# Kernel tuning notes

Hardware: AMD Instinct MI355X
Metric: run time of the kernel (lower is better)

The kernel has to match this reference:

```python
import jax, jax.numpy as jnp
import numpy as np

DIM = 128
H = 8
NEG_SLOPE = 0.2
SCALE = 12.0
N_ITEMS = 81920
E_INT = 163840
N_T = 4096
NUM_NODE = 40000


def _normalize(x, eps=1e-12):
    n = jnp.linalg.norm(x, axis=-1, keepdims=True)
    return x / jnp.maximum(n, eps)


def _gat(feat, src, dst, fc_w, attn_l, attn_r, bias):
    # GATConv with residual (Identity, since in_feats == out_feats) and bias.
    N = feat.shape[0]
    fs = (feat @ fc_w.T).reshape(N, H, DIM)                # [N,H,D]
    el = jnp.einsum('nhd,hd->nh', fs, attn_l)              # [N,H]
    er = jnp.einsum('nhd,hd->nh', fs, attn_r)              # [N,H]
    e = el[src] + er[dst]                                  # u_add_v -> [E,H]
    e = jnp.where(e >= 0, e, NEG_SLOPE * e)                # leaky_relu
    # edge_softmax grouped by destination node
    emax = jax.ops.segment_max(e, dst, num_segments=N)
    ex = jnp.exp(e - emax[dst])
    denom = jax.ops.segment_sum(ex, dst, num_segments=N)
    a = ex / denom[dst]                                    # [E,H]
    # u_mul_e + sum aggregation
    m = fs[src] * a[:, :, None]                            # [E,H,D]
    rst = jax.ops.segment_sum(m, dst, num_segments=N)      # [N,H,D]
    rst = rst + feat[:, None, :] + bias.reshape(1, H, DIM)
    return rst


def setup_inputs() -> dict:
    key = jax.random.key(0)
    ks = jax.random.split(key, 20)
    stdv = 1.0 / np.sqrt(DIM)

    def unif(k, shape):
        return jax.random.uniform(k, shape, jnp.float32, -stdv, stdv)

    return {
        'iid': jax.random.randint(ks[0], (N_ITEMS,), 0, NUM_NODE),
        'tid': jax.random.randint(ks[1], (N_T,), 0, 10),
        'pid': jax.random.randint(ks[2], (N_ITEMS,), 0, 200),
        'src_i': jax.random.randint(ks[3], (E_INT,), 0, N_ITEMS),
        'dst_i': jax.random.randint(ks[4], (E_INT,), 0, N_ITEMS),
        'agg_src': jnp.arange(N_ITEMS),
        'agg_dst': jnp.sort(jax.random.randint(ks[5], (N_ITEMS,), 0, N_T)),
        'last_nodes': jax.random.randint(ks[6], (N_T,), 0, N_ITEMS),
        'emb': unif(ks[7], (NUM_NODE, DIM)),
        'pos_emb': unif(ks[8], (200, DIM)),
        'target_emb': unif(ks[9], (10, DIM)),
        'gat1_fc': unif(ks[10], (H * DIM, DIM)),
        'gat1_al': unif(ks[11], (H, DIM)),
        'gat1_ar': unif(ks[12], (H, DIM)),
        'gat1_b': jnp.zeros((H * DIM,), jnp.float32),
        'gat2_fc': unif(ks[13], (H * DIM, DIM)),
        'gat2_al': unif(ks[14], (H, DIM)),
        'gat2_ar': unif(ks[15], (H, DIM)),
        'gat2_b': jnp.zeros((H * DIM,), jnp.float32),
        'q_w': unif(ks[16], (DIM, 2 * DIM)),
        'fc_sr_w': unif(ks[17], (DIM, 2 * DIM)),
    }


def reference(iid, tid, pid, src_i, dst_i, agg_src, agg_dst, last_nodes,
              emb, pos_emb, target_emb,
              gat1_fc, gat1_al, gat1_ar, gat1_b,
              gat2_fc, gat2_al, gat2_ar, gat2_b,
              q_w, fc_sr_w):
    h_v = _normalize(emb[iid])                              # [N_items, D]
    h_p = pos_emb[pid]                                      # [E_agg, D]
    h_t = target_emb[tid]                                   # [N_T, D]

    # gat1 on interacts; gat2 on reversed interacts; max over heads each
    h1 = _gat(h_v, src_i, dst_i, gat1_fc, gat1_al, gat1_ar, gat1_b).max(axis=1)
    h2 = _gat(h_v, dst_i, src_i, gat2_fc, gat2_al, gat2_ar, gat2_b).max(axis=1)
    h = _normalize(h1 + h2)                                 # [N_items, D]

    # PosAggregator over 'agg' edges (item -> target)
    ft = h[agg_src]                                         # [E_agg, D]
    e = jnp.tanh(jnp.concatenate([ft, h_p], axis=-1) @ q_w.T)
    w = jnp.sum(e * h_t[agg_dst], axis=-1, keepdims=True)   # udf_agg weight
    sr_g = jax.ops.segment_sum(ft * w, agg_dst, num_segments=h_t.shape[0])
    sr_l = h[last_nodes]                                    # last-item features

    sr = jnp.concatenate([sr_g, sr_l], axis=-1) @ fc_sr_w.T
    scores = SCALE * (_normalize(sr) @ _normalize(emb).T)   # [N_T, num_node]
    return scores
```

## Files before the change

kernel.cpp:

```cpp
#include <hip/hip_runtime.h>
#include <stdint.h>

#define DD 128
#define HN 8
#define NITEMS 81920
#define EINT 163840
#define NT 4096
#define NV 40000
#define NVPAD 40064
#define EAGG 81920
#define NEG_SLOPE 0.2f
#define SCALE 12.0f

typedef unsigned short u16;
typedef __attribute__((ext_vector_type(8))) short bf16x8;
typedef __attribute__((ext_vector_type(4))) float f32x4;
typedef __attribute__((ext_vector_type(4))) unsigned short u16x4;

__device__ __forceinline__ float bf2f(unsigned short u){ return __uint_as_float(((unsigned)u)<<16); }
__device__ __forceinline__ unsigned short f2bf(float f){
  unsigned u = __float_as_uint(f);
  u += 0x7fffu + ((u>>16)&1u);
  return (unsigned short)(u>>16);
}

__global__ __launch_bounds__(256) void k_cast3(const float* __restrict__ fc1, const float* __restrict__ fc2,
    const float* __restrict__ qw, const float* __restrict__ fcsr,
    u16* __restrict__ w1, u16* __restrict__ w2, u16* __restrict__ qb, float* __restrict__ fT){
  int i = blockIdx.x*256 + threadIdx.x;
  if (i < 131072) w1[i] = f2bf(fc1[i]);
  else if (i < 262144) w2[i-131072] = f2bf(fc2[i-131072]);
  else if (i < 294912) qb[i-262144] = f2bf(qw[i-262144]);
  else if (i < 327680){
    int j = i - 294912;
    int k = j >> 7, col = j & 127;
    fT[j] = fcsr[(size_t)col*256 + k];
  }
}

__global__ __launch_bounds__(128) void k_prep_u(const float* __restrict__ fc1, const float* __restrict__ al1,
    const float* __restrict__ ar1, const float* __restrict__ fc2, const float* __restrict__ al2,
    const float* __restrict__ ar2, u16* __restrict__ U){
  int r = blockIdx.x, k = threadIdx.x;
  if (r >= 32){ U[(size_t)r*DD + k] = 0; return; }
  int g = r>>3, h = r&7;
  const float* fc = (g>=2)? fc2 : fc1;
  const float* av = (g==0)? al1 : (g==1)? ar1 : (g==2)? al2 : ar2;
  float s = 0.f;
  for (int d=0; d<DD; ++d) s += fc[(size_t)(h*DD+d)*DD + k] * av[h*DD+d];
  U[(size_t)r*DD + k] = f2bf(s);
}

__global__ __launch_bounds__(256) void k_norm(const float* __restrict__ emb, const int* __restrict__ iid,
    u16* __restrict__ nemb, u16* __restrict__ hvb, int* __restrict__ cnt){
  int gi = blockIdx.x*256 + threadIdx.x;
  if (gi < 2*NITEMS) cnt[gi] = 0;
  int w = gi >> 6;
  int lane = gi & 63;
  u16* dst; const float* src;
  if (w < NVPAD){
    dst = nemb + (size_t)w*DD;
    if (w >= NV){ dst[lane*2]=0; dst[lane*2+1]=0; return; }
    src = emb + (size_t)w*DD;
  } else {
    int n = w - NVPAD;
    dst = hvb + (size_t)n*DD;
    src = emb + (size_t)iid[n]*DD;
  }
  float2 v = *(const float2*)(src + lane*2);
  float ss = v.x*v.x + v.y*v.y;
  #pragma unroll
  for (int m=1;m<64;m<<=1) ss += __shfl_xor(ss, m);
  float inv = 1.f / fmaxf(sqrtf(ss), 1e-12f);
  dst[lane*2]   = f2bf(v.x*inv);
  dst[lane*2+1] = f2bf(v.y*inv);
}

template<int OUT_BF16>
__global__ __launch_bounds__(256) void gemm_nt(const u16* __restrict__ A, const u16* __restrict__ B,
                                               void* __restrict__ C, int M, int N, int K,
                                               float alpha, int ldc, int nvalid){
  __shared__ u16 As[128*32];
  __shared__ u16 Bs[128*32];
  int m0 = blockIdx.x*128, n0 = blockIdx.y*128;
  int t = threadIdx.x, lane = t&63, wid = t>>6;
  int wm = wid>>1, wn = wid&1;
  f32x4 zero = {0.f,0.f,0.f,0.f};
  f32x4 acc[4][4];
  #pragma unroll
  for (int i=0;i<4;i++)
    #pragma unroll
    for (int j=0;j<4;j++) acc[i][j] = zero;
  int lr = lane & 15, lk = (lane>>4)*8;
  for (int k0=0; k0<K; k0+=32){
    #pragma unroll
    for (int cc=0; cc<2; ++cc){
      int c = t + cc*256;
      int row = c>>2, col = (c&3)*8;
      *(bf16x8*)(void*)&As[c*8] = *(const bf16x8*)(const void*)&A[(size_t)(m0+row)*K + k0 + col];
      *(bf16x8*)(void*)&Bs[c*8] = *(const bf16x8*)(const void*)&B[(size_t)(n0+row)*K + k0 + col];
    }
    __syncthreads();
    bf16x8 af[4], bfr[4];
    #pragma unroll
    for (int m=0;m<4;m++) af[m]  = *(const bf16x8*)(const void*)&As[(wm*64+m*16+lr)*32 + lk];
    #pragma unroll
    for (int n=0;n<4;n++) bfr[n] = *(const bf16x8*)(const void*)&Bs[(wn*64+n*16+lr)*32 + lk];
    #pragma unroll
    for (int m=0;m<4;m++)
      #pragma unroll
      for (int n=0;n<4;n++)
        acc[m][n] = __builtin_amdgcn_mfma_f32_16x16x32_bf16(af[m], bfr[n], acc[m][n], 0,0,0);
    __syncthreads();
  }
  #pragma unroll
  for (int m=0;m<4;m++)
    #pragma unroll
    for (int n=0;n<4;n++)
      #pragma unroll
      for (int r=0;r<4;r++){
        int row = m0 + wm*64 + m*16 + (lane>>4)*4 + r;
        int col = n0 + wn*64 + n*16 + (lane&15);
        if (col < nvalid){
          float v = acc[m][n][r]*alpha;
          if (OUT_BF16) ((u16*)C)[(size_t)row*ldc + col] = f2bf(v);
          else          ((float*)C)[(size_t)row*ldc + col] = v;
        }
      }
}

__global__ __launch_bounds__(256) void k_deg2(const int* __restrict__ di, const int* __restrict__ si,
                                              int* __restrict__ cnt){
  int i = blockIdx.x*256+threadIdx.x;
  if (i<EINT){ atomicAdd(&cnt[di[i]],1); atomicAdd(&cnt[NITEMS+si[i]],1); }
}

__global__ __launch_bounds__(256) void k_scan_a(int* cnt, int* off, int* bsum, int n){
  __shared__ int buf[256];
  int b = blockIdx.x, t = threadIdx.x, i = b*256+t;
  int v = (i<n)? cnt[i] : 0;
  buf[t] = v; __syncthreads();
  #pragma unroll
  for (int ofs=1; ofs<256; ofs<<=1){
    int x = (t>=ofs)? buf[t-ofs] : 0;
    __syncthreads();
    buf[t] += x;
    __syncthreads();
  }
  if (i<n){ off[i] = buf[t]-v; cnt[i] = 0; }
  if (t==255) bsum[b] = buf[255];
}

__global__ __launch_bounds__(1024) void k_scan_b(int* bsum, int* off, int nb, int n){
  __shared__ int buf[1024];
  int t = threadIdx.x;
  int v = (t<nb)? bsum[t] : 0;
  buf[t]=v; __syncthreads();
  #pragma unroll
  for (int ofs=1; ofs<1024; ofs<<=1){
    int x=(t>=ofs)?buf[t-ofs]:0; __syncthreads(); buf[t]+=x; __syncthreads();
  }
  if (t<nb) bsum[t] = buf[t]-v;
  if (t==1023) off[n] = buf[1023];
}

__global__ __launch_bounds__(256) void k_scan_c(int* __restrict__ off, const int* __restrict__ bsum, int n){
  int i = blockIdx.x*256+threadIdx.x;
  if (i<n) off[i] += bsum[blockIdx.x];
}

__global__ __launch_bounds__(256) void k_scatter2(const int* __restrict__ di, const int* __restrict__ si,
    const int* __restrict__ off, int* __restrict__ cnt, int* __restrict__ sid){
  int i = blockIdx.x*256+threadIdx.x;
  if (i<EINT){
    int a = di[i];         sid[off[a]+atomicAdd(&cnt[a],1)] = si[i];
    int b = NITEMS+si[i];  sid[off[b]+atomicAdd(&cnt[b],1)] = di[i];
  }
}

__global__ __launch_bounds__(256) void k_aw(const int* __restrict__ off, const int* __restrict__ sid,
    const float* __restrict__ ecat, u16* __restrict__ aw){
  int u = blockIdx.x*256 + threadIdx.x;
  if (u >= 2*NITEMS) return;
  int g = (u >= NITEMS) ? 1 : 0;
  int w = u - g*NITEMS;
  int cl = g*16, cr = g*16 + 8;
  float ern[8];
  #pragma unroll
  for (int h=0;h<8;h++) ern[h] = ecat[(size_t)w*32 + cr + h];
  int lo = off[u], hi = off[u+1];
  float den[8];
  #pragma unroll
  for (int h=0;h<8;h++) den[h] = 0.f;
  for (int i=lo;i<hi;++i){
    const float* e = ecat + (size_t)sid[i]*32 + cl;
    #pragma unroll
    for (int h=0;h<8;h++){
      float lv = e[h] + ern[h];
      lv = (lv>=0.f)? lv : NEG_SLOPE*lv;
      den[h] += expf(lv);
    }
  }
  float inv[8];
  #pragma unroll
  for (int h=0;h<8;h++) inv[h] = (den[h]>0.f)? 1.f/den[h] : 0.f;
  for (int i=lo;i<hi;++i){
    const float* e = ecat + (size_t)sid[i]*32 + cl;
    bf16x8 o;
    #pragma unroll
    for (int h=0;h<8;h++){
      float lv = e[h] + ern[h];
      lv = (lv>=0.f)? lv : NEG_SLOPE*lv;
      o[h] = (short)f2bf(expf(lv)*inv[h]);
    }
    *(bf16x8*)(void*)&aw[(size_t)i*8] = o;
  }
}

__global__ __launch_bounds__(512) void k_gatfuse(const int* __restrict__ off, const int* __restrict__ sid,
    const u16* __restrict__ aw, const u16* __restrict__ hvb,
    const u16* __restrict__ wfc1, const u16* __restrict__ wfc2,
    const float* __restrict__ b1, const float* __restrict__ b2,
    u16* __restrict__ hb){
  __shared__ __align__(16) char smem[64*DD*4];
  u16* aggS = (u16*)smem;
  float* F = (float*)smem;
  int n0 = blockIdx.x*64;
  int t = threadIdx.x, lane = t&63, wid = t>>6;
  int lr = lane&15, lq = lane>>4;
  int nd = t>>3, dch = t&7;
  float rm[2][4][4];
  #pragma unroll
  for (int g=0;g<2;g++)
    #pragma unroll
    for (int m=0;m<4;m++)
      #pragma unroll
      for (int r=0;r<4;r++) rm[g][m][r] = -1e30f;

  #pragma unroll
  for (int g=0; g<2; ++g){
    const u16* wfc = g ? wfc2 : wfc1;
    const float* bias = g ? b2 : b1;
    int u = g*NITEMS + n0 + nd;
    int lo = off[u], hi = off[u+1];
    #pragma unroll
    for (int hp=0; hp<4; ++hp){
      float a0[16], a1[16];
      #pragma unroll
      for (int j=0;j<16;j++){ a0[j]=0.f; a1[j]=0.f; }
      for (int i=lo; i<hi; ++i){
        int s = sid[i];
        bf16x8 v0 = *(const bf16x8*)(const void*)&hvb[(size_t)s*DD + dch*16];
        bf16x8 v1 = *(const bf16x8*)(const void*)&hvb[(size_t)s*DD + dch*16 + 8];
        unsigned wp = *(const unsigned*)(const void*)&aw[(size_t)i*8 + 2*hp];
        float w0 = bf2f((u16)(wp & 0xffffu)), w1 = bf2f((u16)(wp >> 16));
        #pragma unroll
        for (int j=0;j<8;j++){
          float f0 = bf2f((u16)v0[j]);
          float f1 = bf2f((u16)v1[j]);
          a0[j] += w0*f0; a0[8+j] += w0*f1;
          a1[j] += w1*f0; a1[8+j] += w1*f1;
        }
      }
      #pragma unroll
      for (int sub=0; sub<2; ++sub){
        int h = 2*hp + sub;
        const float* ap = sub ? a1 : a0;
        __syncthreads();
        {
          bf16x8 o0, o1;
          #pragma unroll
          for (int j=0;j<8;j++){ o0[j] = (short)f2bf(ap[j]); o1[j] = (short)f2bf(ap[8+j]); }
          *(bf16x8*)(void*)&aggS[nd*DD + (((dch*2)   ^ (nd&7))*8)] = o0;
          *(bf16x8*)(void*)&aggS[nd*DD + (((dch*2+1) ^ (nd&7))*8)] = o1;
        }
        __syncthreads();
        f32x4 acc[4];
        #pragma unroll
        for (int m=0;m<4;m++){ f32x4 z={0.f,0.f,0.f,0.f}; acc[m]=z; }
        #pragma unroll
        for (int ks=0; ks<4; ++ks){
          bf16x8 bfr = *(const bf16x8*)(const void*)&wfc[(size_t)(h*DD + wid*16 + lr)*DD + ks*32 + lq*8];
          #pragma unroll
          for (int m=0;m<4;m++){
            int row = m*16 + lr;
            bf16x8 af = *(const bf16x8*)(const void*)&aggS[row*DD + ((((ks*4+lq) ^ (row&7)))*8)];
            acc[m] = __builtin_amdgcn_mfma_f32_16x16x32_bf16(af, bfr, acc[m], 0,0,0);
          }
        }
        float bn = bias[h*DD + wid*16 + lr];
        #pragma unroll
        for (int m=0;m<4;m++)
          #pragma unroll
          for (int r=0;r<4;r++)
            rm[g][m][r] = fmaxf(rm[g][m][r], acc[m][r] + bn);
      }
    }
  }
  __syncthreads();
  #pragma unroll
  for (int m=0;m<4;m++)
    #pragma unroll
    for (int r=0;r<4;r++){
      int row = m*16 + lq*4 + r;
      int col = wid*16 + lr;
      float hvv = bf2f(hvb[(size_t)(n0+row)*DD + col]);
      F[row*DD + col] = rm[0][m][r] + rm[1][m][r] + 2.f*hvv;
    }
  __syncthreads();
  {
    int r8 = t>>3, q = t&7;
    float ss = 0.f;
    #pragma unroll
    for (int j=0;j<16;j+=4){
      float4 v4 = *(const float4*)&F[r8*DD + q*16 + j];
      ss += v4.x*v4.x + v4.y*v4.y + v4.z*v4.z + v4.w*v4.w;
    }
    ss += __shfl_xor(ss,1); ss += __shfl_xor(ss,2); ss += __shfl_xor(ss,4);
    float inv = 1.f/fmaxf(sqrtf(ss),1e-12f);
    #pragma unroll
    for (int j=0;j<16;j+=4){
      float4 v4 = *(const float4*)&F[r8*DD + q*16 + j];
      u16x4 o = {f2bf(v4.x*inv), f2bf(v4.y*inv), f2bf(v4.z*inv), f2bf(v4.w*inv)};
      *(u16x4*)(void*)&hb[(size_t)(n0+r8)*DD + q*16 + j] = o;
    }
  }
}

__global__ __launch_bounds__(256) void k_epw(const int* __restrict__ asrc, const int* __restrict__ pid,
    const int* __restrict__ adst, const int* __restrict__ tid_, const u16* __restrict__ hb,
    const float* __restrict__ pemb, const u16* __restrict__ qwb, const float* __restrict__ temb,
    float* __restrict__ wv){
  __shared__ u16 As[128*32];
  __shared__ u16 Bs[128*32];
  __shared__ float tembS[10*DD];
  __shared__ float wsum[128];
  __shared__ int rowtt[128];
  int m0 = blockIdx.x*128;
  int t = threadIdx.x, lane = t&63, wid = t>>6;
  int wm = wid>>1, wn = wid&1, lr = lane&15, lq = lane>>4;
  for (int i=t; i<10*DD; i+=256) tembS[i] = temb[i];
  if (t < 128){ rowtt[t] = tid_[adst[m0+t]]; wsum[t] = 0.f; }
  f32x4 zero = {0.f,0.f,0.f,0.f};
  f32x4 acc[4][4];
  #pragma unroll
  for (int i=0;i<4;i++)
    #pragma unroll
    for (int j=0;j<4;j++) acc[i][j] = zero;
  for (int k0=0; k0<256; k0+=32){
    #pragma unroll
    for (int cc=0; cc<2; ++cc){
      int c = t + cc*256;
      int row = c>>2;
      int kk = k0 + (c&3)*8;
      bf16x8 av;
      if (k0 < 128){
        av = *(const bf16x8*)(const void*)&hb[(size_t)asrc[m0+row]*DD + kk];
      } else {
        const float* p = pemb + (size_t)pid[m0+row]*DD + (kk-128);
        float4 p0 = *(const float4*)p;
        float4 p1 = *(const float4*)(p+4);
        av[0]=(short)f2bf(p0.x); av[1]=(short)f2bf(p0.y); av[2]=(short)f2bf(p0.z); av[3]=(short)f2bf(p0.w);
        av[4]=(short)f2bf(p1.x); av[5]=(short)f2bf(p1.y); av[6]=(short)f2bf(p1.z); av[7]=(short)f2bf(p1.w);
      }
      *(bf16x8*)(void*)&As[c*8] = av;
      *(bf16x8*)(void*)&Bs[c*8] = *(const bf16x8*)(const void*)&qwb[(size_t)row*256 + kk];
    }
    __syncthreads();
    bf16x8 af[4], bfr[4];
    #pragma unroll
    for (int m=0;m<4;m++) af[m]  = *(const bf16x8*)(const void*)&As[(wm*64+m*16+lr)*32 + lq*8];
    #pragma unroll
    for (int n=0;n<4;n++) bfr[n] = *(const bf16x8*)(const void*)&Bs[(wn*64+n*16+lr)*32 + lq*8];
    #pragma unroll
    for (int m=0;m<4;m++)
      #pragma unroll
      for (int n=0;n<4;n++)
        acc[m][n] = __builtin_amdgcn_mfma_f32_16x16x32_bf16(af[m], bfr[n], acc[m][n], 0,0,0);
    __syncthreads();
  }
  #pragma unroll
  for (int m=0;m<4;m++)
    #pragma unroll
    for (int r=0;r<4;r++){
      int lrow = wm*64 + m*16 + lq*4 + r;
      int tt = rowtt[lrow];
      float p = 0.f;
      #pragma unroll
      for (int n=0;n<4;n++){
        int col = wn*64 + n*16 + lr;
        p += tanhf(acc[m][n][r]) * tembS[tt*DD + col];
      }
      #pragma unroll
      for (int msk=1; msk<16; msk<<=1) p += __shfl_xor(p, msk);
      if (lr==0) atomicAdd(&wsum[lrow], p);
    }
  __syncthreads();
  if (t < 128) wv[m0+t] = wsum[t];
}

__device__ __forceinline__ int lbound(const int* a, int n, int key){
  int lo=0, hi=n;
  while (lo<hi){ int mid=(lo+hi)>>1; if (a[mid]<key) lo=mid+1; else hi=mid; }
  return lo;
}

__global__ __launch_bounds__(256) void k_sr(const u16* __restrict__ hb, const float* __restrict__ w,
    const int* __restrict__ asrc, const int* __restrict__ adst, const int* __restrict__ lastn,
    const float* __restrict__ fcsrT, u16* __restrict__ nsr){
  __shared__ float cat[256];
  __shared__ float red[128];
  __shared__ int lohi[2];
  int t = blockIdx.x, tid = threadIdx.x;
  if (tid == 0){ lohi[0] = lbound(adst, EAGG, t); lohi[1] = lbound(adst, EAGG, t+1); }
  __syncthreads();
  int lo = lohi[0], hi = lohi[1];
  if (tid < DD){
    float a = 0.f;
    for (int i=lo;i<hi;++i) a += bf2f(hb[(size_t)asrc[i]*DD + tid]) * w[i];
    cat[tid] = a;
  } else {
    int d = tid - DD;
    cat[DD + d] = bf2f(hb[(size_t)lastn[t]*DD + d]);
  }
  __syncthreads();
  float s = 0.f;
  if (tid < DD){
    #pragma unroll 8
    for (int k=0;k<256;++k) s += cat[k]*fcsrT[(size_t)k*DD + tid];
    red[tid] = s*s;
  }
  __syncthreads();
  for (int st=64; st>0; st>>=1){
    if (tid < st) red[tid] += red[tid+st];
    __syncthreads();
  }
  if (tid < DD){
    float inv = 1.f/fmaxf(sqrtf(red[0]),1e-12f);
    nsr[(size_t)t*DD + tid] = f2bf(s*inv);
  }
}

__global__ __launch_bounds__(256) void gemm_sc(const u16* __restrict__ A, const u16* __restrict__ B,
                                               float* __restrict__ C){
  __shared__ __align__(16) char smem[16384];
  u16* As = (u16*)smem;
  u16* Bs = As + 4096;
  float* tr = (float*)smem;
  int flat = blockIdx.y*gridDim.x + blockIdx.x;
  int nf = (flat&7)*1252 + (flat>>3);
  int m0 = (nf & 31)*128;
  int n0 = (nf >> 5)*128;
  int t = threadIdx.x, lane = t&63, wid = t>>6;
  int wm = wid>>1, wn = wid&1, lr = lane&15, lq = lane>>4;
  f32x4 zero = {0.f,0.f,0.f,0.f};
  f32x4 acc[4][4];
  #pragma unroll
  for (int i=0;i<4;i++)
    #pragma unroll
    for (int j=0;j<4;j++) acc[i][j] = zero;
  for (int k0=0; k0<DD; k0+=32){
    #pragma unroll
    for (int cc=0; cc<2; ++cc){
      int c = t + cc*256;
      int row = c>>2, col = (c&3)*8;
      *(bf16x8*)(void*)&As[c*8] = *(const bf16x8*)(const void*)&A[(size_t)(m0+row)*DD + k0 + col];
      *(bf16x8*)(void*)&Bs[c*8] = *(const bf16x8*)(const void*)&B[(size_t)(n0+row)*DD + k0 + col];
    }
    __syncthreads();
    bf16x8 af[4], bfr[4];
    #pragma unroll
    for (int m=0;m<4;m++) af[m]  = *(const bf16x8*)(const void*)&As[(wm*64+m*16+lr)*32 + lq*8];
    #pragma unroll
    for (int n=0;n<4;n++) bfr[n] = *(const bf16x8*)(const void*)&Bs[(wn*64+n*16+lr)*32 + lq*8];
    #pragma unroll
    for (int m=0;m<4;m++)
      #pragma unroll
      for (int n=0;n<4;n++)
        acc[m][n] = __builtin_amdgcn_mfma_f32_16x16x32_bf16(af[m], bfr[n], acc[m][n], 0,0,0);
    __syncthreads();
  }
  #pragma unroll
  for (int m=0;m<4;m++){
    #pragma unroll
    for (int n=0;n<4;n++)
      #pragma unroll
      for (int r=0;r<4;r++)
        tr[wid*1024 + (lq*4+r)*64 + n*16 + lr] = acc[m][n][r]*SCALE;
    __syncthreads();
    int row16 = lane>>2, ch = (lane&3)*16;
    int grow = m0 + wm*64 + m*16 + row16;
    int gcol = n0 + wn*64 + ch;
    if (gcol < NV){
      const float* s = &tr[wid*1024 + row16*64 + ch];
      float* d = &C[(size_t)grow*NV + gcol];
      *(float4*)(d)    = *(const float4*)(s);
      *(float4*)(d+4)  = *(const float4*)(s+4);
      *(float4*)(d+8)  = *(const float4*)(s+8);
      *(float4*)(d+12) = *(const float4*)(s+12);
    }
    __syncthreads();
  }
}

extern "C" void kernel_launch(void* const* d_in, const int* in_sizes, int n_in,
                              void* d_out, int out_size, void* d_ws, size_t ws_size,
                              hipStream_t stream){
  (void)in_sizes; (void)n_in; (void)out_size; (void)ws_size;
  const int*   iid   = (const int*)d_in[0];
  const int*   tid_  = (const int*)d_in[1];
  const int*   pid   = (const int*)d_in[2];
  const int*   src_i = (const int*)d_in[3];
  const int*   dst_i = (const int*)d_in[4];
  const int*   asrc  = (const int*)d_in[5];
  const int*   adst  = (const int*)d_in[6];
  const int*   lastn = (const int*)d_in[7];
  const float* emb   = (const float*)d_in[8];
  const float* pemb  = (const float*)d_in[9];
  const float* temb  = (const float*)d_in[10];
  const float* fc1   = (const float*)d_in[11];
  const float* al1   = (const float*)d_in[12];
  const float* ar1   = (const float*)d_in[13];
  const float* b1    = (const float*)d_in[14];
  const float* fc2   = (const float*)d_in[15];
  const float* al2   = (const float*)d_in[16];
  const float* ar2   = (const float*)d_in[17];
  const float* b2    = (const float*)d_in[18];
  const float* qw    = (const float*)d_in[19];
  const float* fcsr  = (const float*)d_in[20];

  char* ws = (char*)d_ws;
  size_t o = 0;
  auto alc = [&](size_t b)->char*{ char* r = ws + o; o += (b + 511) & ~(size_t)511; return r; };
  u16*   hvb  = (u16*)  alc((size_t)NITEMS*DD*2);
  u16*   hb   = (u16*)  alc((size_t)NITEMS*DD*2);
  float* ecat = (float*)alc((size_t)NITEMS*32*4);
  int*   off  = (int*)  alc((size_t)(2*NITEMS+1)*4);
  int*   cnt  = (int*)  alc((size_t)(2*NITEMS)*4);
  int*   bsum = (int*)  alc((size_t)1024*4);
  int*   sid  = (int*)  alc((size_t)(2*EINT)*4);
  u16*   aw   = (u16*)  alc((size_t)(2*EINT)*8*2);
  u16*   wfc1 = (u16*)  alc((size_t)1024*DD*2);
  u16*   wfc2 = (u16*)  alc((size_t)1024*DD*2);
  u16*   qwb  = (u16*)  alc((size_t)DD*256*2);
  float* fT   = (float*)alc((size_t)256*DD*4);
  u16*   Umat = (u16*)  alc((size_t)128*DD*2);
  float* wv   = (float*)alc((size_t)EAGG*4);
  u16*   nsr  = (u16*)  alc((size_t)NT*DD*2);
  u16*   nemb = (u16*)  alc((size_t)NVPAD*DD*2);

  const int N2 = 2*NITEMS;
  const int NB2 = N2/256;

  k_norm<<<(NVPAD+NITEMS)/4, 256, 0, stream>>>(emb, iid, nemb, hvb, cnt);
  k_prep_u<<<128, 128, 0, stream>>>(fc1, al1, ar1, fc2, al2, ar2, Umat);
  k_cast3<<<1280, 256, 0, stream>>>(fc1, fc2, qw, fcsr, wfc1, wfc2, qwb, fT);
  gemm_nt<0><<<dim3(NITEMS/128, 1), 256, 0, stream>>>(hvb, Umat, ecat, NITEMS, 128, DD, 1.f, 32, 32);

  k_deg2<<<(EINT+255)/256, 256, 0, stream>>>(dst_i, src_i, cnt);
  k_scan_a<<<NB2, 256, 0, stream>>>(cnt, off, bsum, N2);
  k_scan_b<<<1, 1024, 0, stream>>>(bsum, off, NB2, N2);
  k_scan_c<<<NB2, 256, 0, stream>>>(off, bsum, N2);
  k_scatter2<<<(EINT+255)/256, 256, 0, stream>>>(dst_i, src_i, off, cnt, sid);

  k_aw<<<N2/256, 256, 0, stream>>>(off, sid, ecat, aw);

  k_gatfuse<<<NITEMS/64, 512, 0, stream>>>(off, sid, aw, hvb, wfc1, wfc2, b1, b2, hb);

  k_epw<<<EAGG/128, 256, 0, stream>>>(asrc, pid, adst, tid_, hb, pemb, qwb, temb, wv);
  k_sr<<<NT, 256, 0, stream>>>(hb, wv, asrc, adst, lastn, fT, nsr);

  gemm_sc<<<dim3(32, NVPAD/128), 256, 0, stream>>>(nsr, nemb, (float*)d_out);
}
```

Before: 674.3 us.

## Gather all heads in one edge pass and halve node tile in fused GAT kernel

The fused GAT kernel now walks each node's edge list once per graph, accumulating all 8 heads together, instead of re-walking it once per head pair (four passes). Per-head aggregates are staged into a padded shared buffer for all heads at once, so the per-head sync pairs disappear. The block tile drops from 64 to 32 nodes with 16 threads per node, doubling the grid. The cost is a larger per-thread accumulator (64 floats), more shared memory and more reloads of weight fragments across blocks.

```diff
diff --git a/kernel.cpp b/kernel.cpp
--- a/kernel.cpp
+++ b/kernel.cpp
@@ -222,108 +222,107 @@
     const u16* __restrict__ wfc1, const u16* __restrict__ wfc2,
     const float* __restrict__ b1, const float* __restrict__ b2,
     u16* __restrict__ hb){
-  __shared__ __align__(16) char smem[64*DD*4];
-  u16* aggS = (u16*)smem;
-  float* F = (float*)smem;
-  int n0 = blockIdx.x*64;
+  __shared__ __align__(16) u16 S[8*32*136];
+  float* F = (float*)S;
+  const int TS = 32*136;
+  int n0 = blockIdx.x*32;
   int t = threadIdx.x, lane = t&63, wid = t>>6;
   int lr = lane&15, lq = lane>>4;
-  int nd = t>>3, dch = t&7;
-  float rm[2][4][4];
+  int nd = t>>4, dch = t&15;
+  int elo[2], ehi[2];
+  #pragma unroll
+  for (int g=0; g<2; ++g){
+    int u = g*NITEMS + n0 + nd;
+    elo[g] = off[u]; ehi[g] = off[u+1];
+  }
+  float rm[2][2][4];
   #pragma unroll
   for (int g=0;g<2;g++)
     #pragma unroll
-    for (int m=0;m<4;m++)
+    for (int m=0;m<2;m++)
       #pragma unroll
       for (int r=0;r<4;r++) rm[g][m][r] = -1e30f;
 
   #pragma unroll
   for (int g=0; g<2; ++g){
+    float a[8][8];
+    #pragma unroll
+    for (int h=0;h<8;h++)
+      #pragma unroll
+      for (int j=0;j<8;j++) a[h][j] = 0.f;
+    for (int i=elo[g]; i<ehi[g]; ++i){
+      int s = sid[i];
+      bf16x8 v  = *(const bf16x8*)(const void*)&hvb[(size_t)s*DD + dch*8];
+      bf16x8 w8 = *(const bf16x8*)(const void*)&aw[(size_t)i*8];
+      float f[8];
+      #pragma unroll
+      for (int j=0;j<8;j++) f[j] = bf2f((u16)v[j]);
+      #pragma unroll
+      for (int h=0;h<8;h++){
+        float wa = bf2f((u16)w8[h]);
+        #pragma unroll
+        for (int j=0;j<8;j++) a[h][j] += wa * f[j];
+      }
+    }
+    __syncthreads();
+    #pragma unroll
+    for (int h=0;h<8;h++){
+      bf16x8 o;
+      #pragma unroll
+      for (int j=0;j<8;j++) o[j] = (short)f2bf(a[h][j]);
+      *(bf16x8*)(void*)&S[h*TS + nd*136 + dch*8] = o;
+    }
+    __syncthreads();
     const u16* wfc = g ? wfc2 : wfc1;
     const float* bias = g ? b2 : b1;
-    int u = g*NITEMS + n0 + nd;
-    int lo = off[u], hi = off[u+1];
-    #pragma unroll
-    for (int hp=0; hp<4; ++hp){
-      float a0[16], a1[16];
-      #pragma unroll
-      for (int j=0;j<16;j++){ a0[j]=0.f; a1[j]=0.f; }
-      for (int i=lo; i<hi; ++i){
-        int s = sid[i];
-        bf16x8 v0 = *(const bf16x8*)(const void*)&hvb[(size_t)s*DD + dch*16];
-        bf16x8 v1 = *(const bf16x8*)(const void*)&hvb[(size_t)s*DD + dch*16 + 8];
-        unsigned wp = *(const unsigned*)(const void*)&aw[(size_t)i*8 + 2*hp];
-        float w0 = bf2f((u16)(wp & 0xffffu)), w1 = bf2f((u16)(wp >> 16));
-        #pragma unroll
-        for (int j=0;j<8;j++){
-          float f0 = bf2f((u16)v0[j]);
-          float f1 = bf2f((u16)v1[j]);
-          a0[j] += w0*f0; a0[8+j] += w0*f1;
-          a1[j] += w1*f0; a1[8+j] += w1*f1;
-        }
+    #pragma unroll
+    for (int h=0; h<8; ++h){
+      bf16x8 bfr[4];
+      #pragma unroll
+      for (int ks=0; ks<4; ++ks)
+        bfr[ks] = *(const bf16x8*)(const void*)&wfc[(size_t)(h*DD + wid*16 + lr)*DD + ks*32 + lq*8];
+      f32x4 acc0 = {0.f,0.f,0.f,0.f}, acc1 = {0.f,0.f,0.f,0.f};
+      #pragma unroll
+      for (int ks=0; ks<4; ++ks){
+        bf16x8 af0 = *(const bf16x8*)(const void*)&S[h*TS + (lr)*136      + ks*32 + lq*8];
+        bf16x8 af1 = *(const bf16x8*)(const void*)&S[h*TS + (16+lr)*136   + ks*32 + lq*8];
+        acc0 = __builtin_amdgcn_mfma_f32_16x16x32_bf16(af0, bfr[ks], acc0, 0,0,0);
+        acc1 = __builtin_amdgcn_mfma_f32_16x16x32_bf16(af1, bfr[ks], acc1, 0,0,0);
       }
-      #pragma unroll
-      for (int sub=0; sub<2; ++sub){
-        int h = 2*hp + sub;
-        const float* ap = sub ? a1 : a0;
-        __syncthreads();
-        {
-          bf16x8 o0, o1;
-          #pragma unroll
-          for (int j=0;j<8;j++){ o0[j] = (short)f2bf(ap[j]); o1[j] = (short)f2bf(ap[8+j]); }
-          *(bf16x8*)(void*)&aggS[nd*DD + (((dch*2)   ^ (nd&7))*8)] = o0;
-          *(bf16x8*)(void*)&aggS[nd*DD + (((dch*2+1) ^ (nd&7))*8)] = o1;
-        }
-        __syncthreads();
-        f32x4 acc[4];
-        #pragma unroll
-        for (int m=0;m<4;m++){ f32x4 z={0.f,0.f,0.f,0.f}; acc[m]=z; }
-        #pragma unroll
-        for (int ks=0; ks<4; ++ks){
-          bf16x8 bfr = *(const bf16x8*)(const void*)&wfc[(size_t)(h*DD + wid*16 + lr)*DD + ks*32 + lq*8];
-          #pragma unroll
-          for (int m=0;m<4;m++){
-            int row = m*16 + lr;
-            bf16x8 af = *(const bf16x8*)(const void*)&aggS[row*DD + ((((ks*4+lq) ^ (row&7)))*8)];
-            acc[m] = __builtin_amdgcn_mfma_f32_16x16x32_bf16(af, bfr, acc[m], 0,0,0);
-          }
-        }
-        float bn = bias[h*DD + wid*16 + lr];
-        #pragma unroll
-        for (int m=0;m<4;m++)
-          #pragma unroll
-          for (int r=0;r<4;r++)
-            rm[g][m][r] = fmaxf(rm[g][m][r], acc[m][r] + bn);
+      float bn = bias[h*DD + wid*16 + lr];
+      #pragma unroll
+      for (int r=0;r<4;r++){
+        rm[g][0][r] = fmaxf(rm[g][0][r], acc0[r] + bn);
+        rm[g][1][r] = fmaxf(rm[g][1][r], acc1[r] + bn);
       }
     }
   }
   __syncthreads();
   #pragma unroll
-  for (int m=0;m<4;m++)
+  for (int m=0;m<2;m++)
     #pragma unroll
     for (int r=0;r<4;r++){
       int row = m*16 + lq*4 + r;
       int col = wid*16 + lr;
       float hvv = bf2f(hvb[(size_t)(n0+row)*DD + col]);
-      F[row*DD + col] = rm[0][m][r] + rm[1][m][r] + 2.f*hvv;
+      F[row*132 + col] = rm[0][m][r] + rm[1][m][r] + 2.f*hvv;
     }
   __syncthreads();
   {
-    int r8 = t>>3, q = t&7;
+    float vals[8];
     float ss = 0.f;
     #pragma unroll
-    for (int j=0;j<16;j+=4){
-      float4 v4 = *(const float4*)&F[r8*DD + q*16 + j];
-      ss += v4.x*v4.x + v4.y*v4.y + v4.z*v4.z + v4.w*v4.w;
-    }
-    ss += __shfl_xor(ss,1); ss += __shfl_xor(ss,2); ss += __shfl_xor(ss,4);
+    for (int j=0;j<8;j++){
+      vals[j] = F[nd*132 + dch*8 + j];
+      ss += vals[j]*vals[j];
+    }
+    ss += __shfl_xor(ss,1); ss += __shfl_xor(ss,2);
+    ss += __shfl_xor(ss,4); ss += __shfl_xor(ss,8);
     float inv = 1.f/fmaxf(sqrtf(ss),1e-12f);
-    #pragma unroll
-    for (int j=0;j<16;j+=4){
-      float4 v4 = *(const float4*)&F[r8*DD + q*16 + j];
-      u16x4 o = {f2bf(v4.x*inv), f2bf(v4.y*inv), f2bf(v4.z*inv), f2bf(v4.w*inv)};
-      *(u16x4*)(void*)&hb[(size_t)(n0+r8)*DD + q*16 + j] = o;
-    }
+    bf16x8 o;
+    #pragma unroll
+    for (int j=0;j<8;j++) o[j] = (short)f2bf(vals[j]*inv);
+    *(bf16x8*)(void*)&hb[(size_t)(n0+nd)*DD + dch*8] = o;
   }
 }
 
@@ -565,7 +564,7 @@
 
   k_aw<<<N2/256, 256, 0, stream>>>(off, sid, ecat, aw);
 
-  k_gatfuse<<<NITEMS/64, 512, 0, stream>>>(off, sid, aw, hvb, wfc1, wfc2, b1, b2, hb);
+  k_gatfuse<<<NITEMS/32, 512, 0, stream>>>(off, sid, aw, hvb, wfc1, wfc2, b1, b2, hb);
 
   k_epw<<<EAGG/128, 256, 0, stream>>>(asrc, pid, adst, tid_, hb, pemb, qwb, temb, wv);
   k_sr<<<NT, 256, 0, stream>>>(hb, wv, asrc, adst, lastn, fT, nsr);
```

Result: faster. 641.6 us (-4.9%).
